# Optimization experiments

Measured on AMD Instinct MI355X. Metric: run time of the kernel, lower is better.

Reference implementation:

```python
import jax, jax.numpy as jnp
import numpy as np


def setup_inputs() -> dict:
    key = jax.random.key(0)
    k1, k2 = jax.random.split(key)
    bsz, n_views, d = 4096, 2, 512
    features = jax.random.normal(k1, (bsz, n_views, d), dtype=jnp.float32)
    labels = jax.random.randint(k2, (bsz,), 0, 100)
    return {"features": features, "labels": labels}


def reference(features, labels):
    # Faithful vectorization of Fourdloss.forward (contrast_mode='all').
    bsz, n_views, d = features.shape
    N = bsz * n_views
    # torch.cat(torch.unbind(features, dim=1), dim=0): view-major stacking
    cf = jnp.transpose(features, (1, 0, 2)).reshape(N, d)  # contrast == anchor feature
    lab = jnp.tile(labels, n_views)                        # labels2[i] = labels[i % bsz]
    same = lab[:, None] == lab[None, :]                    # [N, N]
    neg = ~same                                            # mask2
    negf = neg.astype(jnp.float32)
    # positive mask with diagonal removed (mask * logits_mask)
    pos_mask = same.astype(jnp.float32) * (1.0 - jnp.eye(N, dtype=jnp.float32))

    # pairwise dot products with the hardcoded 0.035 temperature
    D = (cf @ cf.T) / 0.035                                # [N, N], D[m, j] = c_m . a_j / 0.035

    # Inner loop over j: over rows m with labels2[m] != labels2[j],
    # S[j] = sum_m exp(D[m, j] - max_m D[m, j])
    maxd = jnp.max(jnp.where(neg, D, -jnp.inf), axis=0)    # [N], per-column masked max
    z = jnp.where(neg, D - maxd[None, :], 0.0)             # safe: masked entries -> exp(0)*0
    S = jnp.sum(jnp.exp(z) * negf, axis=0)                 # [N]

    # Outer loop over i: sum S[j] over all j that are negatives of i; k = count
    num = negf @ S                                         # negtive_dot_negtive_sum
    negcount = negf.sum(axis=1)                            # negtivesum (k)
    x = num / negcount                                     # [N] (repeated across columns in torch)
    log_prob = -jnp.log(x + 1e-12)                         # constant per row

    pos_count = pos_mask.sum(axis=1)
    mask_sum = jnp.where(pos_count == 0, 1.0, pos_count)
    # (mask * log_prob).sum(1) == log_prob * pos_count since log_prob is row-constant
    pos_logits = -(pos_count * log_prob) / mask_sum
    loss = pos_logits.reshape(n_views, bsz).mean()
    return loss
```

## Files before the change

### kernel.cpp

```cpp
#include <hip/hip_runtime.h>

typedef unsigned short u16;
typedef unsigned int u32;
typedef __attribute__((ext_vector_type(8))) short bfrag;
typedef __attribute__((ext_vector_type(4))) float facc;

#define N 8192
#define DIM 512
#define BM 128
#define BK 32
#define NTILE 2080
#define NPART 64
#define NCLS 100
#define TPX 260

#if __has_builtin(__builtin_amdgcn_exp2f)
#define EXP2(x) __builtin_amdgcn_exp2f(x)
#else
#define EXP2(x) exp2f(x)
#endif

__device__ __forceinline__ u16 f2bf(float f) {
  u32 u = __float_as_uint(f);
  u32 r = u + 0x7fffu + ((u >> 16) & 1u);
  return (u16)(r >> 16);
}
__device__ __forceinline__ float bf2f(u16 h) {
  return __uint_as_float(((u32)h) << 16);
}

__global__ void prep_kernel(const float* __restrict__ F, u16* __restrict__ Ahi,
                            u16* __restrict__ Alo, float* __restrict__ classSum,
                            int* __restrict__ classCnt)
{
  const float sc = sqrtf(1.4426950408889634f / 0.035f);
  int idx = (blockIdx.x * 256 + threadIdx.x) * 4;
  float4 x = *(const float4*)(F + idx);
  float v[4] = {x.x * sc, x.y * sc, x.z * sc, x.w * sc};
  u16 h[4], l[4];
#pragma unroll
  for (int i = 0; i < 4; ++i) {
    h[i] = f2bf(v[i]);
    l[i] = f2bf(v[i] - bf2f(h[i]));
  }
  *(ushort4*)(Ahi + idx) = make_ushort4(h[0], h[1], h[2], h[3]);
  *(ushort4*)(Alo + idx) = make_ushort4(l[0], l[1], l[2], l[3]);
  if (blockIdx.x == 0 && threadIdx.x < NCLS) {
    classSum[threadIdx.x] = 0.f;
    classCnt[threadIdx.x] = 0;
  }
}

__device__ __forceinline__ void stage16(const u16* g, u16* l) {
  __builtin_amdgcn_global_load_lds((const __attribute__((address_space(1))) void*)g,
                                   (__attribute__((address_space(3))) void*)l, 16, 0, 0);
}

__device__ __forceinline__ void mergeMS(float& m, float& s, float m2, float s2) {
  float M = fmaxf(m, m2);
  s = s * EXP2(m - M) + s2 * EXP2(m2 - M);
  m = M;
}

__global__ __launch_bounds__(256, 4) void gram_flash(
    const u16* __restrict__ Ahi, const u16* __restrict__ Alo,
    const int* __restrict__ labels,
    float* __restrict__ m_part, float* __restrict__ s_part)
{
  __shared__ __align__(16) u16 lds[4 * BM * BK];
  u16* lds_ahi = lds;
  u16* lds_alo = lds + BM * BK;
  u16* lds_bhi = lds + 2 * BM * BK;
  u16* lds_blo = lds + 3 * BM * BK;

  const int tid = threadIdx.x;
  const int wave = tid >> 6;
  const int lane = tid & 63;
  const int wr = wave >> 1, wc = wave & 1;
  const int l15 = lane & 15, lg = lane >> 4;

  const int t = (blockIdx.x & 7) * TPX + (blockIdx.x >> 3);
  int SI = 0, base = 0;
  for (;; ++SI) {
    int rowcnt = 36 + (7 - SI) * 64;
    if (t < base + rowcnt) break;
    base += rowcnt;
  }
  const int r = t - base;
  int SJ, li, lj;
  if (r < 36) {
    SJ = SI;
    int a = 0, cum = 0;
    for (;; ++a) { if (r < cum + (8 - a)) break; cum += 8 - a; }
    li = a; lj = a + (r - cum);
  } else {
    int rr = r - 36;
    SJ = SI + 1 + (rr >> 6);
    li = (rr & 63) >> 3;
    lj = rr & 7;
  }
  const int I = SI * 8 + li, J = SJ * 8 + lj;
  const int i0 = I * BM;
  const int j0 = J * BM;

  u32 lr[4];
#pragma unroll
  for (int mi = 0; mi < 4; ++mi) {
    u32 pk = 0;
#pragma unroll
    for (int rg = 0; rg < 4; ++rg) {
      int rr2 = i0 + wr * 64 + mi * 16 + lg * 4 + rg;
      pk |= ((u32)labels[rr2 >> 1] & 0xffu) << (8 * rg);
    }
    lr[mi] = pk;
  }
  int lc[4];
#pragma unroll
  for (int ni = 0; ni < 4; ++ni)
    lc[ni] = labels[(j0 + wc * 64 + ni * 16 + l15) >> 1];

  facc acc[4][4];
#pragma unroll
  for (int a = 0; a < 4; ++a)
#pragma unroll
    for (int b = 0; b < 4; ++b)
      acc[a][b] = (facc){0.f, 0.f, 0.f, 0.f};

  for (int kk = 0; kk < DIM; kk += BK) {
    __syncthreads();
#pragma unroll
    for (int q = 0; q < 2; ++q) {
      const int ci = (wave * 2 + q) * 64 + lane;
      const int L = ci >> 3;
      const int sc2 = ci & 7;
      const int cb = sc2 ^ (L & 7);
      const int row = L * 2 + (cb >> 2);
      const int kc = cb & 3;
      const size_t goffA = (size_t)(i0 + row) * DIM + kk + kc * 8;
      const size_t goffB = (size_t)(j0 + row) * DIM + kk + kc * 8;
      const int lbase = (wave * 2 + q) * 512;
      stage16(Ahi + goffA, lds_ahi + lbase);
      stage16(Alo + goffA, lds_alo + lbase);
      stage16(Ahi + goffB, lds_bhi + lbase);
      stage16(Alo + goffB, lds_blo + lbase);
    }
    asm volatile("s_waitcnt vmcnt(0)" ::: "memory");
    __syncthreads();

    bfrag fah[4], fal[4], fbh[4], fbl[4];
#pragma unroll
    for (int mi = 0; mi < 4; ++mi) {
      const int row = wr * 64 + mi * 16 + l15;
      const int L = row >> 1;
      const int cb = ((row & 1) << 2) | lg;
      const int off = L * 64 + (cb ^ (L & 7)) * 8;
      fah[mi] = *(const bfrag*)(lds_ahi + off);
      fal[mi] = *(const bfrag*)(lds_alo + off);
    }
#pragma unroll
    for (int ni = 0; ni < 4; ++ni) {
      const int row = wc * 64 + ni * 16 + l15;
      const int L = row >> 1;
      const int cb = ((row & 1) << 2) | lg;
      const int off = L * 64 + (cb ^ (L & 7)) * 8;
      fbh[ni] = *(const bfrag*)(lds_bhi + off);
      fbl[ni] = *(const bfrag*)(lds_blo + off);
    }
#pragma unroll
    for (int mi = 0; mi < 4; ++mi)
#pragma unroll
      for (int ni = 0; ni < 4; ++ni)
        acc[mi][ni] = __builtin_amdgcn_mfma_f32_16x16x32_bf16(fah[mi], fbh[ni], acc[mi][ni], 0, 0, 0);
#pragma unroll
    for (int mi = 0; mi < 4; ++mi)
#pragma unroll
      for (int ni = 0; ni < 4; ++ni)
        acc[mi][ni] = __builtin_amdgcn_mfma_f32_16x16x32_bf16(fah[mi], fbl[ni], acc[mi][ni], 0, 0, 0);
#pragma unroll
    for (int mi = 0; mi < 4; ++mi)
#pragma unroll
      for (int ni = 0; ni < 4; ++ni)
        acc[mi][ni] = __builtin_amdgcn_mfma_f32_16x16x32_bf16(fal[mi], fbh[ni], acc[mi][ni], 0, 0, 0);
  }

#pragma unroll
  for (int mi = 0; mi < 4; ++mi)
#pragma unroll
    for (int rg = 0; rg < 4; ++rg) {
      const int labr = (int)((lr[mi] >> (8 * rg)) & 0xffu);
#pragma unroll
      for (int ni = 0; ni < 4; ++ni)
        if (labr == lc[ni]) acc[mi][ni][rg] = -1e30f;
    }

  float rm[16], rs[16];
#pragma unroll
  for (int mi = 0; mi < 4; ++mi)
#pragma unroll
    for (int rg = 0; rg < 4; ++rg) {
      const int si = mi * 4 + rg;
      float m = -1e20f;
#pragma unroll
      for (int ni = 0; ni < 4; ++ni) m = fmaxf(m, acc[mi][ni][rg]);
      float s = 0.f;
#pragma unroll
      for (int ni = 0; ni < 4; ++ni) s += EXP2(acc[mi][ni][rg] - m);
      rm[si] = m; rs[si] = s;
    }
#pragma unroll
  for (int st = 1; st <= 8; st <<= 1)
#pragma unroll
    for (int si = 0; si < 16; ++si)
      mergeMS(rm[si], rs[si], __shfl_xor(rm[si], st, 64), __shfl_xor(rs[si], st, 64));

  float cm[4], cs[4];
#pragma unroll
  for (int ni = 0; ni < 4; ++ni) {
    float m = -1e20f;
#pragma unroll
    for (int mi = 0; mi < 4; ++mi)
#pragma unroll
      for (int rg = 0; rg < 4; ++rg) m = fmaxf(m, acc[mi][ni][rg]);
    float s = 0.f;
#pragma unroll
    for (int mi = 0; mi < 4; ++mi)
#pragma unroll
      for (int rg = 0; rg < 4; ++rg) s += EXP2(acc[mi][ni][rg] - m);
    cm[ni] = m; cs[ni] = s;
  }
#pragma unroll
  for (int st = 16; st <= 32; st <<= 1)
#pragma unroll
    for (int ni = 0; ni < 4; ++ni)
      mergeMS(cm[ni], cs[ni], __shfl_xor(cm[ni], st, 64), __shfl_xor(cs[ni], st, 64));

  float* buf = (float*)lds;
  float* RM = buf;
  float* RS = buf + 256;
  float* CM = buf + 512;
  float* CS = buf + 768;

  __syncthreads();
  if (l15 == 0) {
#pragma unroll
    for (int mi = 0; mi < 4; ++mi)
#pragma unroll
      for (int rg = 0; rg < 4; ++rg) {
        const int idx = wr * 64 + mi * 16 + lg * 4 + rg;
        RM[wc * 128 + idx] = rm[mi * 4 + rg];
        RS[wc * 128 + idx] = rs[mi * 4 + rg];
      }
  }
  if (lg == 0 && I != J) {
#pragma unroll
    for (int ni = 0; ni < 4; ++ni) {
      const int c = wc * 64 + ni * 16 + l15;
      CM[wr * 128 + c] = cm[ni];
      CS[wr * 128 + c] = cs[ni];
    }
  }
  __syncthreads();

  if (tid < 128) {
    float m = RM[tid], s = RS[tid];
    mergeMS(m, s, RM[128 + tid], RS[128 + tid]);
    m_part[(size_t)J * N + i0 + tid] = m;
    s_part[(size_t)J * N + i0 + tid] = s;
  } else if (I != J) {
    const int c = tid - 128;
    float m = CM[c], s = CS[c];
    mergeMS(m, s, CM[128 + c], CS[128 + c]);
    m_part[(size_t)I * N + j0 + c] = m;
    s_part[(size_t)I * N + j0 + c] = s;
  }
}

__global__ void combine_kernel(const float* __restrict__ m_part,
                               const float* __restrict__ s_part,
                               const int* __restrict__ labels,
                               float* __restrict__ classSum,
                               int* __restrict__ classCnt)
{
  int j = blockIdx.x * 256 + threadIdx.x;
  float M = -1e20f;
  for (int p = 0; p < NPART; ++p) M = fmaxf(M, m_part[p * N + j]);
  float S = 0.f;
  for (int p = 0; p < NPART; ++p)
    S += s_part[p * N + j] * EXP2(m_part[p * N + j] - M);
  int c = labels[j >> 1];
  atomicAdd(&classSum[c], S);
  atomicAdd(&classCnt[c], 1);
}

__global__ void final_kernel(const float* __restrict__ classSum,
                             const int* __restrict__ classCnt,
                             float* __restrict__ out)
{
  __shared__ float red[128];
  int t = threadIdx.x;
  float total = 0.f;
  for (int c = 0; c < NCLS; ++c) total += classSum[c];
  float term = 0.f;
  if (t < NCLS) {
    int cnt = classCnt[t];
    if (cnt > 0) {
      float x = (total - classSum[t]) / (float)(N - cnt) + 1e-12f;
      term = (float)cnt * logf(x);
    }
  }
  red[t] = term;
  __syncthreads();
  for (int s = 64; s > 0; s >>= 1) {
    if (t < s) red[t] += red[t + s];
    __syncthreads();
  }
  if (t == 0) out[0] = red[0] / (float)N;
}

extern "C" void kernel_launch(void* const* d_in, const int* in_sizes, int n_in,
                              void* d_out, int out_size, void* d_ws, size_t ws_size,
                              hipStream_t stream)
{
  (void)in_sizes; (void)n_in; (void)out_size; (void)ws_size;
  const float* F = (const float*)d_in[0];
  const int* labels = (const int*)d_in[1];
  float* out = (float*)d_out;

  char* ws = (char*)d_ws;
  u16* Ahi = (u16*)ws;
  u16* Alo = (u16*)(ws + (size_t)N * DIM * 2);
  float* m_part = (float*)(ws + (size_t)N * DIM * 4);
  float* s_part = m_part + (size_t)NPART * N;
  float* classSum = s_part + (size_t)NPART * N;
  int* classCnt = (int*)(classSum + NCLS);

  prep_kernel<<<(N * DIM) / 1024, 256, 0, stream>>>(F, Ahi, Alo, classSum, classCnt);
  gram_flash<<<NTILE, 256, 0, stream>>>(Ahi, Alo, labels, m_part, s_part);
  combine_kernel<<<N / 256, 256, 0, stream>>>(m_part, s_part, labels, classSum, classCnt);
  final_kernel<<<1, 128, 0, stream>>>(classSum, classCnt, out);
}
```

Before: 220.4 us.

## Double-buffer LDS tiles in gram kernel and parallelize partial combine

The gram kernel now keeps two LDS buffers and issues the global-to-LDS loads for the next K slice before running the MFMAs on the current one, so load latency overlaps with compute. Launch bounds drop from 4 to 2 blocks per CU to allow for the doubled shared memory. The combine kernel splits the 64 partitions across 4 waves with an online max/sum merge through shared memory, using 4x more blocks. The risks are lower occupancy and the single barrier per iteration, which with vmcnt(0) still waits on the prefetch at the end of each step.

```diff
diff --git a/kernel.cpp b/kernel.cpp
--- a/kernel.cpp
+++ b/kernel.cpp
@@ -9,6 +9,7 @@
 #define DIM 512
 #define BM 128
 #define BK 32
+#define NK (DIM / BK)
 #define NTILE 2080
 #define NPART 64
 #define NCLS 100
@@ -62,17 +63,12 @@
   m = M;
 }
 
-__global__ __launch_bounds__(256, 4) void gram_flash(
+__global__ __launch_bounds__(256, 2) void gram_flash(
     const u16* __restrict__ Ahi, const u16* __restrict__ Alo,
     const int* __restrict__ labels,
     float* __restrict__ m_part, float* __restrict__ s_part)
 {
-  __shared__ __align__(16) u16 lds[4 * BM * BK];
-  u16* lds_ahi = lds;
-  u16* lds_alo = lds + BM * BK;
-  u16* lds_bhi = lds + 2 * BM * BK;
-  u16* lds_blo = lds + 3 * BM * BK;
-
+  __shared__ __align__(16) u16 lds[2][4 * BM * BK];
   const int tid = threadIdx.x;
   const int wave = tid >> 6;
   const int lane = tid & 63;
@@ -126,8 +122,12 @@
     for (int b = 0; b < 4; ++b)
       acc[a][b] = (facc){0.f, 0.f, 0.f, 0.f};
 
-  for (int kk = 0; kk < DIM; kk += BK) {
-    __syncthreads();
+  auto STAGE = [&](int kk, int b) {
+    u16* d_ahi = &lds[b][0];
+    u16* d_alo = &lds[b][BM * BK];
+    u16* d_bhi = &lds[b][2 * BM * BK];
+    u16* d_blo = &lds[b][3 * BM * BK];
+    const int k0 = kk * BK;
 #pragma unroll
     for (int q = 0; q < 2; ++q) {
       const int ci = (wave * 2 + q) * 64 + lane;
@@ -136,16 +136,28 @@
       const int cb = sc2 ^ (L & 7);
       const int row = L * 2 + (cb >> 2);
       const int kc = cb & 3;
-      const size_t goffA = (size_t)(i0 + row) * DIM + kk + kc * 8;
-      const size_t goffB = (size_t)(j0 + row) * DIM + kk + kc * 8;
+      const size_t goffA = (size_t)(i0 + row) * DIM + k0 + kc * 8;
+      const size_t goffB = (size_t)(j0 + row) * DIM + k0 + kc * 8;
       const int lbase = (wave * 2 + q) * 512;
-      stage16(Ahi + goffA, lds_ahi + lbase);
-      stage16(Alo + goffA, lds_alo + lbase);
-      stage16(Ahi + goffB, lds_bhi + lbase);
-      stage16(Alo + goffB, lds_blo + lbase);
-    }
-    asm volatile("s_waitcnt vmcnt(0)" ::: "memory");
-    __syncthreads();
+      stage16(Ahi + goffA, d_ahi + lbase);
+      stage16(Alo + goffA, d_alo + lbase);
+      stage16(Ahi + goffB, d_bhi + lbase);
+      stage16(Alo + goffB, d_blo + lbase);
+    }
+  };
+
+  STAGE(0, 0);
+  asm volatile("s_waitcnt vmcnt(0)" ::: "memory");
+  __syncthreads();
+
+  for (int k = 0; k < NK; ++k) {
+    const int cur = k & 1;
+    if (k + 1 < NK) STAGE(k + 1, cur ^ 1);
+
+    const u16* lb_ahi = &lds[cur][0];
+    const u16* lb_alo = &lds[cur][BM * BK];
+    const u16* lb_bhi = &lds[cur][2 * BM * BK];
+    const u16* lb_blo = &lds[cur][3 * BM * BK];
 
     bfrag fah[4], fal[4], fbh[4], fbl[4];
 #pragma unroll
@@ -154,8 +166,8 @@
       const int L = row >> 1;
       const int cb = ((row & 1) << 2) | lg;
       const int off = L * 64 + (cb ^ (L & 7)) * 8;
-      fah[mi] = *(const bfrag*)(lds_ahi + off);
-      fal[mi] = *(const bfrag*)(lds_alo + off);
+      fah[mi] = *(const bfrag*)(lb_ahi + off);
+      fal[mi] = *(const bfrag*)(lb_alo + off);
     }
 #pragma unroll
     for (int ni = 0; ni < 4; ++ni) {
@@ -163,8 +175,8 @@
       const int L = row >> 1;
       const int cb = ((row & 1) << 2) | lg;
       const int off = L * 64 + (cb ^ (L & 7)) * 8;
-      fbh[ni] = *(const bfrag*)(lds_bhi + off);
-      fbl[ni] = *(const bfrag*)(lds_blo + off);
+      fbh[ni] = *(const bfrag*)(lb_bhi + off);
+      fbl[ni] = *(const bfrag*)(lb_blo + off);
     }
 #pragma unroll
     for (int mi = 0; mi < 4; ++mi)
@@ -181,6 +193,9 @@
 #pragma unroll
       for (int ni = 0; ni < 4; ++ni)
         acc[mi][ni] = __builtin_amdgcn_mfma_f32_16x16x32_bf16(fal[mi], fbh[ni], acc[mi][ni], 0, 0, 0);
+
+    asm volatile("s_waitcnt vmcnt(0)" ::: "memory");
+    __syncthreads();
   }
 
 #pragma unroll
@@ -234,7 +249,7 @@
     for (int ni = 0; ni < 4; ++ni)
       mergeMS(cm[ni], cs[ni], __shfl_xor(cm[ni], st, 64), __shfl_xor(cs[ni], st, 64));
 
-  float* buf = (float*)lds;
+  float* buf = (float*)&lds[0][0];
   float* RM = buf;
   float* RS = buf + 256;
   float* CM = buf + 512;
@@ -281,15 +296,22 @@
                                float* __restrict__ classSum,
                                int* __restrict__ classCnt)
 {
-  int j = blockIdx.x * 256 + threadIdx.x;
-  float M = -1e20f;
-  for (int p = 0; p < NPART; ++p) M = fmaxf(M, m_part[p * N + j]);
-  float S = 0.f;
-  for (int p = 0; p < NPART; ++p)
-    S += s_part[p * N + j] * EXP2(m_part[p * N + j] - M);
-  int c = labels[j >> 1];
-  atomicAdd(&classSum[c], S);
-  atomicAdd(&classCnt[c], 1);
+  __shared__ float MB[4][64], SB[4][64];
+  const int jloc = threadIdx.x & 63;
+  const int pc = threadIdx.x >> 6;
+  const int j = blockIdx.x * 64 + jloc;
+  float M = -1e20f, S = 0.f;
+  for (int p = pc * 16; p < pc * 16 + 16; ++p)
+    mergeMS(M, S, m_part[(size_t)p * N + j], s_part[(size_t)p * N + j]);
+  MB[pc][jloc] = M; SB[pc][jloc] = S;
+  __syncthreads();
+  if (pc == 0) {
+#pragma unroll
+    for (int q = 1; q < 4; ++q) mergeMS(M, S, MB[q][jloc], SB[q][jloc]);
+    int c = labels[j >> 1];
+    atomicAdd(&classSum[c], S);
+    atomicAdd(&classCnt[c], 1);
+  }
 }
 
 __global__ void final_kernel(const float* __restrict__ classSum,
@@ -336,6 +358,6 @@
 
   prep_kernel<<<(N * DIM) / 1024, 256, 0, stream>>>(F, Ahi, Alo, classSum, classCnt);
   gram_flash<<<NTILE, 256, 0, stream>>>(Ahi, Alo, labels, m_part, s_part);
-  combine_kernel<<<N / 256, 256, 0, stream>>>(m_part, s_part, labels, classSum, classCnt);
+  combine_kernel<<<N / 64, 256, 0, stream>>>(m_part, s_part, labels, classSum, classCnt);
   final_kernel<<<1, 128, 0, stream>>>(classSum, classCnt, out);
 }
```

Measured after the change: 217.9 us. No clear change (-1.2%).

## Make gram kernel persistent over multiple tiles and parallelize combine over partitions

Applied to the files above, without the earlier changes.

The gram kernel now launches 1024 blocks, and each block loops over 2 or 3 consecutive upper-triangle tiles instead of one block per tile. The epilogue reduction buffer moves to a separate shared array so it no longer aliases the staging tiles. The combine kernel splits the 64 partials per column across 4 waves using an online max/sum merge in shared memory. The goal is to cut block launch and tail overhead and to give more parallelism to the combine step, at the cost of uneven per-block work and extra shared memory.

```diff
diff --git a/kernel.cpp b/kernel.cpp
--- a/kernel.cpp
+++ b/kernel.cpp
@@ -9,10 +9,12 @@
 #define DIM 512
 #define BM 128
 #define BK 32
+#define NK (DIM / BK)
 #define NTILE 2080
 #define NPART 64
 #define NCLS 100
 #define TPX 260
+#define NBLK 1024
 
 #if __has_builtin(__builtin_amdgcn_exp2f)
 #define EXP2(x) __builtin_amdgcn_exp2f(x)
@@ -68,6 +70,7 @@
     float* __restrict__ m_part, float* __restrict__ s_part)
 {
   __shared__ __align__(16) u16 lds[4 * BM * BK];
+  __shared__ float mbuf[1024];
   u16* lds_ahi = lds;
   u16* lds_alo = lds + BM * BK;
   u16* lds_bhi = lds + 2 * BM * BK;
@@ -79,199 +82,206 @@
   const int wr = wave >> 1, wc = wave & 1;
   const int l15 = lane & 15, lg = lane >> 4;
 
-  const int t = (blockIdx.x & 7) * TPX + (blockIdx.x >> 3);
-  int SI = 0, base = 0;
-  for (;; ++SI) {
-    int rowcnt = 36 + (7 - SI) * 64;
-    if (t < base + rowcnt) break;
-    base += rowcnt;
-  }
-  const int r = t - base;
-  int SJ, li, lj;
-  if (r < 36) {
-    SJ = SI;
-    int a = 0, cum = 0;
-    for (;; ++a) { if (r < cum + (8 - a)) break; cum += 8 - a; }
-    li = a; lj = a + (r - cum);
-  } else {
-    int rr = r - 36;
-    SJ = SI + 1 + (rr >> 6);
-    li = (rr & 63) >> 3;
-    lj = rr & 7;
-  }
-  const int I = SI * 8 + li, J = SJ * 8 + lj;
-  const int i0 = I * BM;
-  const int j0 = J * BM;
-
-  u32 lr[4];
-#pragma unroll
-  for (int mi = 0; mi < 4; ++mi) {
-    u32 pk = 0;
-#pragma unroll
-    for (int rg = 0; rg < 4; ++rg) {
-      int rr2 = i0 + wr * 64 + mi * 16 + lg * 4 + rg;
-      pk |= ((u32)labels[rr2 >> 1] & 0xffu) << (8 * rg);
-    }
-    lr[mi] = pk;
-  }
-  int lc[4];
-#pragma unroll
-  for (int ni = 0; ni < 4; ++ni)
-    lc[ni] = labels[(j0 + wc * 64 + ni * 16 + l15) >> 1];
-
-  facc acc[4][4];
-#pragma unroll
-  for (int a = 0; a < 4; ++a)
-#pragma unroll
-    for (int b = 0; b < 4; ++b)
-      acc[a][b] = (facc){0.f, 0.f, 0.f, 0.f};
-
-  for (int kk = 0; kk < DIM; kk += BK) {
+  const int x = blockIdx.x & 7;
+  const int lb = blockIdx.x >> 3;
+  int tstart, tcnt;
+  if (lb < 4) { tstart = x * TPX + lb * 3;            tcnt = 3; }
+  else        { tstart = x * TPX + 12 + (lb - 4) * 2; tcnt = 2; }
+
+  for (int u = 0; u < tcnt; ++u) {
+    const int t = tstart + u;
+    int SI = 0, base = 0;
+    for (;; ++SI) {
+      int rowcnt = 36 + (7 - SI) * 64;
+      if (t < base + rowcnt) break;
+      base += rowcnt;
+    }
+    const int r = t - base;
+    int SJ, li, lj;
+    if (r < 36) {
+      SJ = SI;
+      int a = 0, cum = 0;
+      for (;; ++a) { if (r < cum + (8 - a)) break; cum += 8 - a; }
+      li = a; lj = a + (r - cum);
+    } else {
+      int rr = r - 36;
+      SJ = SI + 1 + (rr >> 6);
+      li = (rr & 63) >> 3;
+      lj = rr & 7;
+    }
+    const int I = SI * 8 + li, J = SJ * 8 + lj;
+    const int i0 = I * BM;
+    const int j0 = J * BM;
+
+    u32 lr[4];
+#pragma unroll
+    for (int mi = 0; mi < 4; ++mi) {
+      u32 pk = 0;
+#pragma unroll
+      for (int rg = 0; rg < 4; ++rg) {
+        int rr2 = i0 + wr * 64 + mi * 16 + lg * 4 + rg;
+        pk |= ((u32)labels[rr2 >> 1] & 0xffu) << (8 * rg);
+      }
+      lr[mi] = pk;
+    }
+    int lc[4];
+#pragma unroll
+    for (int ni = 0; ni < 4; ++ni)
+      lc[ni] = labels[(j0 + wc * 64 + ni * 16 + l15) >> 1];
+
+    facc acc[4][4];
+#pragma unroll
+    for (int a = 0; a < 4; ++a)
+#pragma unroll
+      for (int b = 0; b < 4; ++b)
+        acc[a][b] = (facc){0.f, 0.f, 0.f, 0.f};
+
+    for (int kk = 0; kk < DIM; kk += BK) {
+      __syncthreads();
+#pragma unroll
+      for (int q = 0; q < 2; ++q) {
+        const int ci = (wave * 2 + q) * 64 + lane;
+        const int L = ci >> 3;
+        const int sc2 = ci & 7;
+        const int cb = sc2 ^ (L & 7);
+        const int row = L * 2 + (cb >> 2);
+        const int kc = cb & 3;
+        const size_t goffA = (size_t)(i0 + row) * DIM + kk + kc * 8;
+        const size_t goffB = (size_t)(j0 + row) * DIM + kk + kc * 8;
+        const int lbase = (wave * 2 + q) * 512;
+        stage16(Ahi + goffA, lds_ahi + lbase);
+        stage16(Alo + goffA, lds_alo + lbase);
+        stage16(Ahi + goffB, lds_bhi + lbase);
+        stage16(Alo + goffB, lds_blo + lbase);
+      }
+      asm volatile("s_waitcnt vmcnt(0)" ::: "memory");
+      __syncthreads();
+
+      bfrag fah[4], fal[4], fbh[4], fbl[4];
+#pragma unroll
+      for (int mi = 0; mi < 4; ++mi) {
+        const int row = wr * 64 + mi * 16 + l15;
+        const int L = row >> 1;
+        const int cb = ((row & 1) << 2) | lg;
+        const int off = L * 64 + (cb ^ (L & 7)) * 8;
+        fah[mi] = *(const bfrag*)(lds_ahi + off);
+        fal[mi] = *(const bfrag*)(lds_alo + off);
+      }
+#pragma unroll
+      for (int ni = 0; ni < 4; ++ni) {
+        const int row = wc * 64 + ni * 16 + l15;
+        const int L = row >> 1;
+        const int cb = ((row & 1) << 2) | lg;
+        const int off = L * 64 + (cb ^ (L & 7)) * 8;
+        fbh[ni] = *(const bfrag*)(lds_bhi + off);
+        fbl[ni] = *(const bfrag*)(lds_blo + off);
+      }
+#pragma unroll
+      for (int mi = 0; mi < 4; ++mi)
+#pragma unroll
+        for (int ni = 0; ni < 4; ++ni)
+          acc[mi][ni] = __builtin_amdgcn_mfma_f32_16x16x32_bf16(fah[mi], fbh[ni], acc[mi][ni], 0, 0, 0);
+#pragma unroll
+      for (int mi = 0; mi < 4; ++mi)
+#pragma unroll
+        for (int ni = 0; ni < 4; ++ni)
+          acc[mi][ni] = __builtin_amdgcn_mfma_f32_16x16x32_bf16(fah[mi], fbl[ni], acc[mi][ni], 0, 0, 0);
+#pragma unroll
+      for (int mi = 0; mi < 4; ++mi)
+#pragma unroll
+        for (int ni = 0; ni < 4; ++ni)
+          acc[mi][ni] = __builtin_amdgcn_mfma_f32_16x16x32_bf16(fal[mi], fbh[ni], acc[mi][ni], 0, 0, 0);
+    }
+
+#pragma unroll
+    for (int mi = 0; mi < 4; ++mi)
+#pragma unroll
+      for (int rg = 0; rg < 4; ++rg) {
+        const int labr = (int)((lr[mi] >> (8 * rg)) & 0xffu);
+#pragma unroll
+        for (int ni = 0; ni < 4; ++ni)
+          if (labr == lc[ni]) acc[mi][ni][rg] = -1e30f;
+      }
+
+    float rm[16], rs[16];
+#pragma unroll
+    for (int mi = 0; mi < 4; ++mi)
+#pragma unroll
+      for (int rg = 0; rg < 4; ++rg) {
+        const int si = mi * 4 + rg;
+        float m = -1e20f;
+#pragma unroll
+        for (int ni = 0; ni < 4; ++ni) m = fmaxf(m, acc[mi][ni][rg]);
+        float s = 0.f;
+#pragma unroll
+        for (int ni = 0; ni < 4; ++ni) s += EXP2(acc[mi][ni][rg] - m);
+        rm[si] = m; rs[si] = s;
+      }
+#pragma unroll
+    for (int st = 1; st <= 8; st <<= 1)
+#pragma unroll
+      for (int si = 0; si < 16; ++si)
+        mergeMS(rm[si], rs[si], __shfl_xor(rm[si], st, 64), __shfl_xor(rs[si], st, 64));
+
+    float cm[4], cs[4];
+#pragma unroll
+    for (int ni = 0; ni < 4; ++ni) {
+      float m = -1e20f;
+#pragma unroll
+      for (int mi = 0; mi < 4; ++mi)
+#pragma unroll
+        for (int rg = 0; rg < 4; ++rg) m = fmaxf(m, acc[mi][ni][rg]);
+      float s = 0.f;
+#pragma unroll
+      for (int mi = 0; mi < 4; ++mi)
+#pragma unroll
+        for (int rg = 0; rg < 4; ++rg) s += EXP2(acc[mi][ni][rg] - m);
+      cm[ni] = m; cs[ni] = s;
+    }
+#pragma unroll
+    for (int st = 16; st <= 32; st <<= 1)
+#pragma unroll
+      for (int ni = 0; ni < 4; ++ni)
+        mergeMS(cm[ni], cs[ni], __shfl_xor(cm[ni], st, 64), __shfl_xor(cs[ni], st, 64));
+
+    float* RM = mbuf;
+    float* RS = mbuf + 256;
+    float* CM = mbuf + 512;
+    float* CS = mbuf + 768;
+
     __syncthreads();
-#pragma unroll
-    for (int q = 0; q < 2; ++q) {
-      const int ci = (wave * 2 + q) * 64 + lane;
-      const int L = ci >> 3;
-      const int sc2 = ci & 7;
-      const int cb = sc2 ^ (L & 7);
-      const int row = L * 2 + (cb >> 2);
-      const int kc = cb & 3;
-      const size_t goffA = (size_t)(i0 + row) * DIM + kk + kc * 8;
-      const size_t goffB = (size_t)(j0 + row) * DIM + kk + kc * 8;
-      const int lbase = (wave * 2 + q) * 512;
-      stage16(Ahi + goffA, lds_ahi + lbase);
-      stage16(Alo + goffA, lds_alo + lbase);
-      stage16(Ahi + goffB, lds_bhi + lbase);
-      stage16(Alo + goffB, lds_blo + lbase);
-    }
-    asm volatile("s_waitcnt vmcnt(0)" ::: "memory");
+    if (l15 == 0) {
+#pragma unroll
+      for (int mi = 0; mi < 4; ++mi)
+#pragma unroll
+        for (int rg = 0; rg < 4; ++rg) {
+          const int idx = wr * 64 + mi * 16 + lg * 4 + rg;
+          RM[wc * 128 + idx] = rm[mi * 4 + rg];
+          RS[wc * 128 + idx] = rs[mi * 4 + rg];
+        }
+    }
+    if (lg == 0 && I != J) {
+#pragma unroll
+      for (int ni = 0; ni < 4; ++ni) {
+        const int c = wc * 64 + ni * 16 + l15;
+        CM[wr * 128 + c] = cm[ni];
+        CS[wr * 128 + c] = cs[ni];
+      }
+    }
     __syncthreads();
 
-    bfrag fah[4], fal[4], fbh[4], fbl[4];
-#pragma unroll
-    for (int mi = 0; mi < 4; ++mi) {
-      const int row = wr * 64 + mi * 16 + l15;
-      const int L = row >> 1;
-      const int cb = ((row & 1) << 2) | lg;
-      const int off = L * 64 + (cb ^ (L & 7)) * 8;
-      fah[mi] = *(const bfrag*)(lds_ahi + off);
-      fal[mi] = *(const bfrag*)(lds_alo + off);
-    }
-#pragma unroll
-    for (int ni = 0; ni < 4; ++ni) {
-      const int row = wc * 64 + ni * 16 + l15;
-      const int L = row >> 1;
-      const int cb = ((row & 1) << 2) | lg;
-      const int off = L * 64 + (cb ^ (L & 7)) * 8;
-      fbh[ni] = *(const bfrag*)(lds_bhi + off);
-      fbl[ni] = *(const bfrag*)(lds_blo + off);
-    }
-#pragma unroll
-    for (int mi = 0; mi < 4; ++mi)
-#pragma unroll
-      for (int ni = 0; ni < 4; ++ni)
-        acc[mi][ni] = __builtin_amdgcn_mfma_f32_16x16x32_bf16(fah[mi], fbh[ni], acc[mi][ni], 0, 0, 0);
-#pragma unroll
-    for (int mi = 0; mi < 4; ++mi)
-#pragma unroll
-      for (int ni = 0; ni < 4; ++ni)
-        acc[mi][ni] = __builtin_amdgcn_mfma_f32_16x16x32_bf16(fah[mi], fbl[ni], acc[mi][ni], 0, 0, 0);
-#pragma unroll
-    for (int mi = 0; mi < 4; ++mi)
-#pragma unroll
-      for (int ni = 0; ni < 4; ++ni)
-        acc[mi][ni] = __builtin_amdgcn_mfma_f32_16x16x32_bf16(fal[mi], fbh[ni], acc[mi][ni], 0, 0, 0);
-  }
-
-#pragma unroll
-  for (int mi = 0; mi < 4; ++mi)
-#pragma unroll
-    for (int rg = 0; rg < 4; ++rg) {
-      const int labr = (int)((lr[mi] >> (8 * rg)) & 0xffu);
-#pragma unroll
-      for (int ni = 0; ni < 4; ++ni)
-        if (labr == lc[ni]) acc[mi][ni][rg] = -1e30f;
-    }
-
-  float rm[16], rs[16];
-#pragma unroll
-  for (int mi = 0; mi < 4; ++mi)
-#pragma unroll
-    for (int rg = 0; rg < 4; ++rg) {
-      const int si = mi * 4 + rg;
-      float m = -1e20f;
-#pragma unroll
-      for (int ni = 0; ni < 4; ++ni) m = fmaxf(m, acc[mi][ni][rg]);
-      float s = 0.f;
-#pragma unroll
-      for (int ni = 0; ni < 4; ++ni) s += EXP2(acc[mi][ni][rg] - m);
-      rm[si] = m; rs[si] = s;
-    }
-#pragma unroll
-  for (int st = 1; st <= 8; st <<= 1)
-#pragma unroll
-    for (int si = 0; si < 16; ++si)
-      mergeMS(rm[si], rs[si], __shfl_xor(rm[si], st, 64), __shfl_xor(rs[si], st, 64));
-
-  float cm[4], cs[4];
-#pragma unroll
-  for (int ni = 0; ni < 4; ++ni) {
-    float m = -1e20f;
-#pragma unroll
-    for (int mi = 0; mi < 4; ++mi)
-#pragma unroll
-      for (int rg = 0; rg < 4; ++rg) m = fmaxf(m, acc[mi][ni][rg]);
-    float s = 0.f;
-#pragma unroll
-    for (int mi = 0; mi < 4; ++mi)
-#pragma unroll
-      for (int rg = 0; rg < 4; ++rg) s += EXP2(acc[mi][ni][rg] - m);
-    cm[ni] = m; cs[ni] = s;
-  }
-#pragma unroll
-  for (int st = 16; st <= 32; st <<= 1)
-#pragma unroll
-    for (int ni = 0; ni < 4; ++ni)
-      mergeMS(cm[ni], cs[ni], __shfl_xor(cm[ni], st, 64), __shfl_xor(cs[ni], st, 64));
-
-  float* buf = (float*)lds;
-  float* RM = buf;
-  float* RS = buf + 256;
-  float* CM = buf + 512;
-  float* CS = buf + 768;
-
-  __syncthreads();
-  if (l15 == 0) {
-#pragma unroll
-    for (int mi = 0; mi < 4; ++mi)
-#pragma unroll
-      for (int rg = 0; rg < 4; ++rg) {
-        const int idx = wr * 64 + mi * 16 + lg * 4 + rg;
-        RM[wc * 128 + idx] = rm[mi * 4 + rg];
-        RS[wc * 128 + idx] = rs[mi * 4 + rg];
-      }
-  }
-  if (lg == 0 && I != J) {
-#pragma unroll
-    for (int ni = 0; ni < 4; ++ni) {
-      const int c = wc * 64 + ni * 16 + l15;
-      CM[wr * 128 + c] = cm[ni];
-      CS[wr * 128 + c] = cs[ni];
-    }
-  }
-  __syncthreads();
-
-  if (tid < 128) {
-    float m = RM[tid], s = RS[tid];
-    mergeMS(m, s, RM[128 + tid], RS[128 + tid]);
-    m_part[(size_t)J * N + i0 + tid] = m;
-    s_part[(size_t)J * N + i0 + tid] = s;
-  } else if (I != J) {
-    const int c = tid - 128;
-    float m = CM[c], s = CS[c];
-    mergeMS(m, s, CM[128 + c], CS[128 + c]);
-    m_part[(size_t)I * N + j0 + c] = m;
-    s_part[(size_t)I * N + j0 + c] = s;
+    if (tid < 128) {
+      float m = RM[tid], s = RS[tid];
+      mergeMS(m, s, RM[128 + tid], RS[128 + tid]);
+      m_part[(size_t)J * N + i0 + tid] = m;
+      s_part[(size_t)J * N + i0 + tid] = s;
+    } else if (I != J) {
+      const int c = tid - 128;
+      float m = CM[c], s = CS[c];
+      mergeMS(m, s, CM[128 + c], CS[128 + c]);
+      m_part[(size_t)I * N + j0 + c] = m;
+      s_part[(size_t)I * N + j0 + c] = s;
+    }
   }
 }
 
@@ -281,15 +291,22 @@
                                float* __restrict__ classSum,
                                int* __restrict__ classCnt)
 {
-  int j = blockIdx.x * 256 + threadIdx.x;
-  float M = -1e20f;
-  for (int p = 0; p < NPART; ++p) M = fmaxf(M, m_part[p * N + j]);
-  float S = 0.f;
-  for (int p = 0; p < NPART; ++p)
-    S += s_part[p * N + j] * EXP2(m_part[p * N + j] - M);
-  int c = labels[j >> 1];
-  atomicAdd(&classSum[c], S);
-  atomicAdd(&classCnt[c], 1);
+  __shared__ float MB[4][64], SB[4][64];
+  const int jloc = threadIdx.x & 63;
+  const int pc = threadIdx.x >> 6;
+  const int j = blockIdx.x * 64 + jloc;
+  float M = -1e20f, S = 0.f;
+  for (int p = pc * 16; p < pc * 16 + 16; ++p)
+    mergeMS(M, S, m_part[(size_t)p * N + j], s_part[(size_t)p * N + j]);
+  MB[pc][jloc] = M; SB[pc][jloc] = S;
+  __syncthreads();
+  if (pc == 0) {
+#pragma unroll
+    for (int q = 1; q < 4; ++q) mergeMS(M, S, MB[q][jloc], SB[q][jloc]);
+    int c = labels[j >> 1];
+    atomicAdd(&classSum[c], S);
+    atomicAdd(&classCnt[c], 1);
+  }
 }
 
 __global__ void final_kernel(const float* __restrict__ classSum,
@@ -335,7 +352,7 @@
   int* classCnt = (int*)(classSum + NCLS);
 
   prep_kernel<<<(N * DIM) / 1024, 256, 0, stream>>>(F, Ahi, Alo, classSum, classCnt);
-  gram_flash<<<NTILE, 256, 0, stream>>>(Ahi, Alo, labels, m_part, s_part);
-  combine_kernel<<<N / 256, 256, 0, stream>>>(m_part, s_part, labels, classSum, classCnt);
+  gram_flash<<<NBLK, 256, 0, stream>>>(Ahi, Alo, labels, m_part, s_part);
+  combine_kernel<<<N / 64, 256, 0, stream>>>(m_part, s_part, labels, classSum, classCnt);
   final_kernel<<<1, 128, 0, stream>>>(classSum, classCnt, out);
 }
```

After: 216.1 us. 1.02x faster.
